# Kernel tuning notes

Hardware: AMD Instinct MI355X
Metric: run time of the kernel (lower is better)

Reference implementation:

```python
import jax, jax.numpy as jnp
import numpy as np

N, K, D_IN, D_H, D_A, N_CLS = 8192, 10, 1024, 512, 256, 4


def setup_inputs() -> dict:
    key = jax.random.key(0)
    ks = jax.random.split(key, 20)
    def lin(k, fan_in, shape):
        return jax.random.normal(k, shape, dtype=jnp.float32) / np.sqrt(fan_in)
    return {
        "x_path": jax.random.normal(ks[0], (N, D_IN), dtype=jnp.float32),
        "cluster_id": jax.random.randint(ks[1], (N,), 0, K),
        # per-cluster phi MLP (Linear 1024->512, ReLU, Linear 512->512, ReLU); dropout = eval identity
        "W1": lin(ks[2], D_IN, (K, D_IN, D_H)), "b1": jnp.zeros((K, D_H), jnp.float32),
        "W2": lin(ks[3], D_H, (K, D_H, D_H)), "b2": jnp.zeros((K, D_H), jnp.float32),
        # attention_net fc: Linear 512->512 + ReLU
        "fc_W": lin(ks[4], D_H, (D_H, D_H)), "fc_b": jnp.zeros((D_H,), jnp.float32),
        # Attn_Net_Gated: a=tanh(Va), b=sigmoid(Vb), A=(a*b)@Vc
        "Va": lin(ks[5], D_H, (D_H, D_A)), "ba": jnp.zeros((D_A,), jnp.float32),
        "Vb": lin(ks[6], D_H, (D_H, D_A)), "bb": jnp.zeros((D_A,), jnp.float32),
        "Vc": lin(ks[7], D_A, (D_A, 1)), "bc": jnp.zeros((1,), jnp.float32),
        # rho: Linear 512->256 + ReLU
        "rho_W": lin(ks[8], D_H, (D_H, D_A)), "rho_b": jnp.zeros((D_A,), jnp.float32),
        # classifier: Linear 256->4
        "cls_W": lin(ks[9], D_A, (D_A, N_CLS)), "cls_b": jnp.zeros((N_CLS,), jnp.float32),
    }


def reference(x_path, cluster_id, W1, b1, W2, b2, fc_W, fc_b,
              Va, ba, Vb, bb, Vc, bc, rho_W, rho_b, cls_W, cls_b):
    # mask[k, n] = 1 if patch n belongs to cluster k
    mask = (cluster_id[None, :] == jnp.arange(K)[:, None]).astype(x_path.dtype)  # [K, N]

    # per-cluster 2-layer MLP applied to all patches, masked mean-pool (= AdaptiveAvgPool1d(1))
    def phi(W1i, b1i, W2i, b2i):
        h = jax.nn.relu(x_path @ W1i + b1i)          # [N, 512]
        return jax.nn.relu(h @ W2i + b2i)            # [N, 512]
    y = jax.vmap(phi)(W1, b1, W2, b2)                # [K, N, 512]
    cnt = mask.sum(axis=1)                           # [K]
    pooled = jnp.einsum('kn,knd->kd', mask, y) / jnp.maximum(cnt, 1.0)[:, None]  # [K, 512]
    # empty cluster -> zeros (matches torch.zeros((1,512)) branch since b terms are zero via where)
    pooled = jnp.where(cnt[:, None] > 0, pooled, 0.0)

    # attention_net: fc + gated attention
    h = jax.nn.relu(pooled @ fc_W + fc_b)            # [K, 512]
    a = jnp.tanh(h @ Va + ba)                        # [K, 256]
    b = jax.nn.sigmoid(h @ Vb + bb)                  # [K, 256]
    A = (a * b) @ Vc + bc                            # [K, 1]
    A = jax.nn.softmax(A.T, axis=1)                  # [1, K]
    h_path = A @ h                                   # [1, 512]
    h_path = jax.nn.relu(h_path @ rho_W + rho_b)[0]  # [256]
    logits = (h_path @ cls_W + cls_b)[None, :]       # [1, 4]
    Y_hat = jnp.argmax(logits, axis=1, keepdims=True)
    hazards = jax.nn.sigmoid(logits)
    S = jnp.cumprod(1.0 - hazards, axis=1)
    return hazards, S, Y_hat
```

## Files before the change

kernel.cpp:

```cpp
#include <hip/hip_runtime.h>
#include <math.h>

#define NPATCH 8192
#define KC     10
#define DIN    1024
#define DH     512
#define DA     256
#define NCLS   4

#define TM  32
#define LDA 520

typedef unsigned short u16;
typedef short bf16x8 __attribute__((ext_vector_type(8)));
typedef float f32x4  __attribute__((ext_vector_type(4)));

#define OFF_CNT   0
#define OFF_IDX   64
#define OFF_PSUM  327744
#define OFF_H     348224
#define OFF_S     368704
#define OFF_H2    368768
#define OFF_W1P   369792
#define OFF_W2P   10855552
#define OFF_XB    16098432
#define OFF_H1    32875648

__device__ __forceinline__ u16 f2bf(float f) {
  union { float f; unsigned u; } v; v.f = f;
  unsigned r = (v.u + 0x7fffu + ((v.u >> 16) & 1u)) >> 16;
  return (u16)r;
}

struct __align__(8) U16x4 { u16 x, y, z, w; };

__device__ __forceinline__ void async16(const void* gp, void* lp) {
  __builtin_amdgcn_global_load_lds(
      (const __attribute__((address_space(1))) void*)gp,
      (__attribute__((address_space(3))) void*)lp, 16, 0, 0);
}

#define W1_TILES (KC * (DIN / 32) * (DH / 32))
#define W2_TILES (KC * (DH / 32) * (DH / 32))
#define NB_BUCKET 32
#define NB_XB     2048
#define NB_PREP   (NB_BUCKET + W1_TILES + W2_TILES + NB_XB)

__global__ __launch_bounds__(256) void prep_kernel(
    const int* __restrict__ cid, int* __restrict__ cnt,
    int* __restrict__ idxlist, const float* __restrict__ W1,
    const float* __restrict__ W2, u16* __restrict__ W1p,
    u16* __restrict__ W2p, const float* __restrict__ x,
    u16* __restrict__ xb, float* __restrict__ psum,
    float* __restrict__ sstore) {
  int b = blockIdx.x, t = threadIdx.x;
  if (b < NB_BUCKET) {
    int g = b * 256 + t;
    if (g < KC * DH) psum[g] = 0.f;
    if (g < KC) sstore[g] = 0.f;
    __shared__ int lcnt[KC], lbase[KC];
    if (t < KC) lcnt[t] = 0;
    __syncthreads();
    int n = b * 256 + t;
    int k = cid[n];
    int myoff = atomicAdd(&lcnt[k], 1);
    __syncthreads();
    if (t < KC) lbase[t] = atomicAdd(&cnt[t], lcnt[t]);
    __syncthreads();
    idxlist[k * NPATCH + lbase[k] + myoff] = n;
  } else if (b < NB_BUCKET + W1_TILES + W2_TILES) {
    __shared__ u16 tile[32][33];
    int bb = b - NB_BUCKET;
    const float* src;
    u16* dst;
    if (bb < W1_TILES) {
      int k = bb / 512, rem = bb % 512;
      int kb = rem / 16, n0 = (rem % 16) * 32;
      src = W1 + (size_t)k * DIN * DH + (size_t)kb * 32 * DH + n0;
      dst = W1p + (((size_t)(k * 32 + kb) * 512 + n0) * 32);
    } else {
      int b2 = bb - W1_TILES;
      int k = b2 / 256, rem = b2 % 256;
      int kb = rem / 16, n0 = (rem % 16) * 32;
      src = W2 + (size_t)k * DH * DH + (size_t)kb * 32 * DH + n0;
      dst = W2p + (((size_t)(k * 16 + kb) * 512 + n0) * 32);
    }
    {
      int ki = t >> 3, n4 = (t & 7) * 4;
      float4 v = *(const float4*)&src[(size_t)ki * DH + n4];
      tile[ki][n4 + 0] = f2bf(v.x);
      tile[ki][n4 + 1] = f2bf(v.y);
      tile[ki][n4 + 2] = f2bf(v.z);
      tile[ki][n4 + 3] = f2bf(v.w);
    }
    __syncthreads();
    {
      int n = t >> 3, ki = (t & 7) * 4;
      U16x4 o = {tile[ki + 0][n], tile[ki + 1][n], tile[ki + 2][n],
                 tile[ki + 3][n]};
      *(U16x4*)&dst[(size_t)n * 32 + ki] = o;
    }
  } else {
    int cb = b - (NB_BUCKET + W1_TILES + W2_TILES);
    size_t basei = (size_t)cb * 4096;
#pragma unroll
    for (int i = 0; i < 4; ++i) {
      size_t off = basei + (size_t)i * 1024 + (size_t)t * 4;
      float4 v = *(const float4*)(x + off);
      U16x4 o = {f2bf(v.x), f2bf(v.y), f2bf(v.z), f2bf(v.w)};
      *(U16x4*)(xb + off) = o;
    }
  }
}

__global__ __launch_bounds__(256) void phi1_kernel(
    const u16* __restrict__ xb, const u16* __restrict__ W1p,
    const float* __restrict__ b1, const int* __restrict__ cnt,
    const int* __restrict__ idxlist, u16* __restrict__ h1) {
  const int k = blockIdx.y;
  const int base = blockIdx.x * TM;
  const int nq = blockIdx.z;
  const int cntk = cnt[k];
  if (base >= cntk) return;

  const int tid = threadIdx.x;
  const int w = tid >> 6, lane = tid & 63;
  const int quad = lane >> 4, l16 = lane & 15;

  __shared__ __align__(16) u16 A_sh[TM * LDA];
  __shared__ int ridx[TM];
  if (tid < TM) {
    int r = base + tid;
    ridx[tid] = (r < cntk) ? idxlist[k * NPATCH + r] : -1;
  }
  __syncthreads();

  const f32x4 zero4 = {0.f, 0.f, 0.f, 0.f};
  f32x4 acc[2][2];
#pragma unroll
  for (int m = 0; m < 2; ++m)
#pragma unroll
    for (int nt = 0; nt < 2; ++nt) acc[m][nt] = zero4;

  for (int kh = 0; kh < 2; ++kh) {
    if (kh) __syncthreads();
    for (int rr = 0; rr < 8; ++rr) {
      int r = w * 8 + rr;
      int src = ridx[r];
      if (src >= 0) {
        async16(xb + (size_t)src * DIN + kh * 512 + lane * 8, &A_sh[r * LDA]);
      } else {
        bf16x8 z = {0, 0, 0, 0, 0, 0, 0, 0};
        *(bf16x8*)&A_sh[r * LDA + lane * 8] = z;
      }
    }
    __syncthreads();

    const u16* wb = W1p + ((size_t)(k * 32 + kh * 16) * 512 +
                           (nq * 128 + w * 32 + l16)) * 32 + quad * 8;
    bf16x8 B[2][8];
#pragma unroll
    for (int s = 0; s < 4; ++s)
#pragma unroll
      for (int nt = 0; nt < 2; ++nt)
        B[0][s * 2 + nt] = *(const bf16x8*)(wb + (size_t)s * 16384 + nt * 512);
#pragma unroll
    for (int g = 0; g < 4; ++g) {
      const int cur = g & 1, nxt = cur ^ 1;
      if (g < 3) {
#pragma unroll
        for (int s = 0; s < 4; ++s)
#pragma unroll
          for (int nt = 0; nt < 2; ++nt)
            B[nxt][s * 2 + nt] = *(const bf16x8*)(
                wb + (size_t)((g + 1) * 4 + s) * 16384 + nt * 512);
      }
#pragma unroll
      for (int s = 0; s < 4; ++s) {
        const int ks = g * 4 + s;
        bf16x8 af0 = *(const bf16x8*)&A_sh[l16 * LDA + ks * 32 + quad * 8];
        bf16x8 af1 =
            *(const bf16x8*)&A_sh[(16 + l16) * LDA + ks * 32 + quad * 8];
#pragma unroll
        for (int nt = 0; nt < 2; ++nt) {
          acc[0][nt] = __builtin_amdgcn_mfma_f32_16x16x32_bf16(
              af0, B[cur][s * 2 + nt], acc[0][nt], 0, 0, 0);
          acc[1][nt] = __builtin_amdgcn_mfma_f32_16x16x32_bf16(
              af1, B[cur][s * 2 + nt], acc[1][nt], 0, 0, 0);
        }
      }
    }
  }

  __syncthreads();
#pragma unroll
  for (int m = 0; m < 2; ++m)
#pragma unroll
    for (int nt = 0; nt < 2; ++nt) {
      int c = w * 32 + nt * 16 + l16;
      float bias = b1[k * DH + nq * 128 + c];
#pragma unroll
      for (int r = 0; r < 4; ++r) {
        int row = m * 16 + quad * 4 + r;
        A_sh[row * 136 + c] = f2bf(fmaxf(acc[m][nt][r] + bias, 0.f));
      }
    }
  __syncthreads();
  {
    int row = tid >> 3, seg = tid & 7;
    int n = ridx[row];
    if (n >= 0) {
      u16* dst = h1 + (size_t)n * DH + nq * 128 + seg * 16;
#pragma unroll
      for (int j = 0; j < 2; ++j)
        *(bf16x8*)(dst + j * 8) =
            *(const bf16x8*)&A_sh[row * 136 + seg * 16 + j * 8];
    }
  }
}

__global__ __launch_bounds__(256) void phi2_kernel(
    const u16* __restrict__ h1, const u16* __restrict__ W2p,
    const float* __restrict__ b2, const int* __restrict__ cnt,
    const int* __restrict__ idxlist, float* __restrict__ psum) {
  const int k = blockIdx.y;
  const int base = blockIdx.x * TM;
  const int nq = blockIdx.z;
  const int cntk = cnt[k];
  if (base >= cntk) return;

  const int tid = threadIdx.x;
  const int w = tid >> 6, lane = tid & 63;
  const int quad = lane >> 4, l16 = lane & 15;

  __shared__ __align__(16) u16 H_sh[TM * LDA];
  __shared__ int ridx[TM];
  if (tid < TM) {
    int r = base + tid;
    ridx[tid] = (r < cntk) ? idxlist[k * NPATCH + r] : -1;
  }
  __syncthreads();

  for (int rr = 0; rr < 8; ++rr) {
    int r = w * 8 + rr;
    int src = ridx[r];
    if (src >= 0) {
      async16(h1 + (size_t)src * DH + lane * 8, &H_sh[r * LDA]);
    } else {
      bf16x8 z = {0, 0, 0, 0, 0, 0, 0, 0};
      *(bf16x8*)&H_sh[r * LDA + lane * 8] = z;
    }
  }
  __syncthreads();

  const f32x4 zero4 = {0.f, 0.f, 0.f, 0.f};
  f32x4 acc[2][2];
#pragma unroll
  for (int m = 0; m < 2; ++m)
#pragma unroll
    for (int nt = 0; nt < 2; ++nt) acc[m][nt] = zero4;

  const u16* wb = W2p + ((size_t)(k * 16) * 512 +
                         (nq * 128 + w * 32 + l16)) * 32 + quad * 8;
  bf16x8 B[2][8];
#pragma unroll
  for (int s = 0; s < 4; ++s)
#pragma unroll
    for (int nt = 0; nt < 2; ++nt)
      B[0][s * 2 + nt] = *(const bf16x8*)(wb + (size_t)s * 16384 + nt * 512);
#pragma unroll
  for (int g = 0; g < 4; ++g) {
    const int cur = g & 1, nxt = cur ^ 1;
    if (g < 3) {
#pragma unroll
      for (int s = 0; s < 4; ++s)
#pragma unroll
        for (int nt = 0; nt < 2; ++nt)
          B[nxt][s * 2 + nt] = *(const bf16x8*)(
              wb + (size_t)((g + 1) * 4 + s) * 16384 + nt * 512);
    }
#pragma unroll
    for (int s = 0; s < 4; ++s) {
      const int ks = g * 4 + s;
      bf16x8 af0 = *(const bf16x8*)&H_sh[l16 * LDA + ks * 32 + quad * 8];
      bf16x8 af1 =
          *(const bf16x8*)&H_sh[(16 + l16) * LDA + ks * 32 + quad * 8];
#pragma unroll
      for (int nt = 0; nt < 2; ++nt) {
        acc[0][nt] = __builtin_amdgcn_mfma_f32_16x16x32_bf16(
            af0, B[cur][s * 2 + nt], acc[0][nt], 0, 0, 0);
        acc[1][nt] = __builtin_amdgcn_mfma_f32_16x16x32_bf16(
            af1, B[cur][s * 2 + nt], acc[1][nt], 0, 0, 0);
      }
    }
  }

  float vmask[2][4];
#pragma unroll
  for (int m = 0; m < 2; ++m)
#pragma unroll
    for (int r = 0; r < 4; ++r)
      vmask[m][r] = (ridx[m * 16 + quad * 4 + r] >= 0) ? 1.f : 0.f;

#pragma unroll
  for (int nt = 0; nt < 2; ++nt) {
    int col = nq * 128 + w * 32 + nt * 16 + l16;
    float bias = b2[k * DH + col];
    float s = 0.f;
#pragma unroll
    for (int m = 0; m < 2; ++m)
#pragma unroll
      for (int r = 0; r < 4; ++r)
        s += vmask[m][r] * fmaxf(acc[m][nt][r] + bias, 0.f);
    s += __shfl_xor(s, 16, 64);
    s += __shfl_xor(s, 32, 64);
    if (quad == 0) atomicAdd(&psum[k * DH + col], s);
  }
}

__global__ __launch_bounds__(256) void fc_kernel(
    const float* __restrict__ psum, const int* __restrict__ cnt,
    const float* __restrict__ fcW, const float* __restrict__ fcb,
    float* __restrict__ hstore) {
  __shared__ float p_sh[KC * DH];
  __shared__ float invs[16];
  __shared__ float red[16 * 16 * KC];
  const int tid = threadIdx.x;
  const int j0 = blockIdx.x * 16;
  const int j = tid & 15, dq = tid >> 4;

  if (tid < KC) {
    int c = cnt[tid];
    invs[tid] = (c > 0) ? 1.f / (float)c : 0.f;
  }
  __syncthreads();
#pragma unroll
  for (int it = 0; it < KC * DH / 256; ++it) {
    int e = it * 256 + tid;
    p_sh[e] = psum[e] * invs[e >> 9];
  }
  __syncthreads();

  float acc[KC];
#pragma unroll
  for (int k = 0; k < KC; ++k) acc[k] = 0.f;
#pragma unroll 8
  for (int i = 0; i < 32; ++i) {
    int ii = (i + dq) & 31;
    int d = dq * 32 + ii;
    float wv = fcW[(size_t)d * DH + j0 + j];
#pragma unroll
    for (int k = 0; k < KC; ++k)
      acc[k] = fmaf(p_sh[k * DH + d], wv, acc[k]);
  }
#pragma unroll
  for (int k = 0; k < KC; ++k) red[(dq * 16 + j) * KC + k] = acc[k];
  __syncthreads();
  if (tid < 16 * KC) {
    int jj = tid / KC, k = tid % KC;
    float s = 0.f;
#pragma unroll
    for (int q = 0; q < 16; ++q) s += red[(q * 16 + jj) * KC + k];
    hstore[k * DH + j0 + jj] = fmaxf(s + fcb[j0 + jj], 0.f);
  }
}

__global__ __launch_bounds__(256) void attn_kernel(
    const float* __restrict__ hstore, const float* __restrict__ Va,
    const float* __restrict__ ba, const float* __restrict__ Vb,
    const float* __restrict__ bb_, const float* __restrict__ Vc,
    float* __restrict__ sstore) {
  __shared__ float h_sh[KC * DH];
  __shared__ float reda[16 * 16 * KC];
  __shared__ float redb[16 * 16 * KC];
  __shared__ float gred[16 * KC];
  const int tid = threadIdx.x;
  const int j0 = blockIdx.x * 16;
  const int j = tid & 15, dq = tid >> 4;

#pragma unroll
  for (int it = 0; it < KC * DH / 256; ++it) {
    int e = it * 256 + tid;
    h_sh[e] = hstore[e];
  }
  __syncthreads();

  float sa[KC], sb[KC];
#pragma unroll
  for (int k = 0; k < KC; ++k) { sa[k] = 0.f; sb[k] = 0.f; }
#pragma unroll 8
  for (int i = 0; i < 32; ++i) {
    int ii = (i + dq) & 31;
    int d = dq * 32 + ii;
    float va = Va[(size_t)d * DA + j0 + j];
    float vb = Vb[(size_t)d * DA + j0 + j];
#pragma unroll
    for (int k = 0; k < KC; ++k) {
      float h = h_sh[k * DH + d];
      sa[k] = fmaf(h, va, sa[k]);
      sb[k] = fmaf(h, vb, sb[k]);
    }
  }
#pragma unroll
  for (int k = 0; k < KC; ++k) {
    reda[(dq * 16 + j) * KC + k] = sa[k];
    redb[(dq * 16 + j) * KC + k] = sb[k];
  }
  __syncthreads();
  if (tid < 16 * KC) {
    int jj = tid / KC, k = tid % KC;
    float ta = 0.f, tb = 0.f;
#pragma unroll
    for (int q = 0; q < 16; ++q) {
      ta += reda[(q * 16 + jj) * KC + k];
      tb += redb[(q * 16 + jj) * KC + k];
    }
    float a = tanhf(ta + ba[j0 + jj]);
    float b = 1.f / (1.f + expf(-(tb + bb_[j0 + jj])));
    gred[jj * KC + k] = a * b * Vc[j0 + jj];
  }
  __syncthreads();
  if (tid < KC) {
    float s = 0.f;
#pragma unroll
    for (int jj = 0; jj < 16; ++jj) s += gred[jj * KC + tid];
    atomicAdd(&sstore[tid], s);
  }
}

__global__ __launch_bounds__(256) void rho_kernel(
    const float* __restrict__ hstore, const float* __restrict__ sstore,
    const float* __restrict__ rhoW, const float* __restrict__ rhob,
    float* __restrict__ h2g) {
  __shared__ float ws_sh[KC];
  __shared__ float hp_sh[DH];
  __shared__ float red[8 * 32];
  const int tid = threadIdx.x;
  const int j0 = blockIdx.x * 32;
  const int j = tid & 31, dq = tid >> 5;

  if (tid == 0) {
    float sv[KC], m = -1e30f;
#pragma unroll
    for (int k = 0; k < KC; ++k) { sv[k] = sstore[k]; m = fmaxf(m, sv[k]); }
    float Z = 0.f;
#pragma unroll
    for (int k = 0; k < KC; ++k) { sv[k] = expf(sv[k] - m); Z += sv[k]; }
    float invZ = 1.f / Z;
#pragma unroll
    for (int k = 0; k < KC; ++k) ws_sh[k] = sv[k] * invZ;
  }
  __syncthreads();
#pragma unroll
  for (int it = 0; it < 2; ++it) {
    int d = it * 256 + tid;
    float s = 0.f;
#pragma unroll
    for (int k = 0; k < KC; ++k) s = fmaf(ws_sh[k], hstore[k * DH + d], s);
    hp_sh[d] = s;
  }
  __syncthreads();

  float acc = 0.f;
#pragma unroll 8
  for (int i = 0; i < 64; ++i) {
    int d = dq * 64 + i;
    acc = fmaf(hp_sh[d], rhoW[(size_t)d * DA + j0 + j], acc);
  }
  red[dq * 32 + j] = acc;
  __syncthreads();
  if (tid < 32) {
    float s = 0.f;
#pragma unroll
    for (int q = 0; q < 8; ++q) s += red[q * 32 + tid];
    h2g[j0 + tid] = fmaxf(s + rhob[j0 + tid], 0.f);
  }
}

__global__ __launch_bounds__(256) void cls_kernel(
    const float* __restrict__ h2g, const float* __restrict__ clsW,
    const float* __restrict__ clsb, float* __restrict__ out) {
  __shared__ float rd[NCLS][256];
  const int tid = threadIdx.x;
  float h = h2g[tid];
#pragma unroll
  for (int c = 0; c < NCLS; ++c) rd[c][tid] = h * clsW[tid * NCLS + c];
  __syncthreads();
  for (int s = 128; s > 0; s >>= 1) {
    if (tid < s) {
#pragma unroll
      for (int c = 0; c < NCLS; ++c) rd[c][tid] += rd[c][tid + s];
    }
    __syncthreads();
  }
  if (tid == 0) {
    float lg[NCLS], hz[NCLS];
    int best = 0;
#pragma unroll
    for (int c = 0; c < NCLS; ++c) {
      lg[c] = rd[c][0] + clsb[c];
      hz[c] = 1.f / (1.f + expf(-lg[c]));
      if (lg[c] > lg[best]) best = c;
    }
    float S = 1.f;
#pragma unroll
    for (int c = 0; c < NCLS; ++c) out[c] = hz[c];
#pragma unroll
    for (int c = 0; c < NCLS; ++c) {
      S *= (1.f - hz[c]);
      out[NCLS + c] = S;
    }
    out[2 * NCLS] = (float)best;
  }
}

extern "C" void kernel_launch(void* const* d_in, const int* in_sizes, int n_in,
                              void* d_out, int out_size, void* d_ws,
                              size_t ws_size, hipStream_t stream) {
  const float* x    = (const float*)d_in[0];
  const int*   cid  = (const int*)d_in[1];
  const float* W1   = (const float*)d_in[2];
  const float* b1   = (const float*)d_in[3];
  const float* W2   = (const float*)d_in[4];
  const float* b2   = (const float*)d_in[5];
  const float* fcW  = (const float*)d_in[6];
  const float* fcb  = (const float*)d_in[7];
  const float* Va   = (const float*)d_in[8];
  const float* ba   = (const float*)d_in[9];
  const float* Vb   = (const float*)d_in[10];
  const float* bb_  = (const float*)d_in[11];
  const float* Vc   = (const float*)d_in[12];
  const float* rhoW = (const float*)d_in[14];
  const float* rhob = (const float*)d_in[15];
  const float* clsW = (const float*)d_in[16];
  const float* clsb = (const float*)d_in[17];
  float* out = (float*)d_out;

  char* ws = (char*)d_ws;
  int*   cnt     = (int*)(ws + OFF_CNT);
  int*   idxlist = (int*)(ws + OFF_IDX);
  float* psum    = (float*)(ws + OFF_PSUM);
  float* hstore  = (float*)(ws + OFF_H);
  float* sstore  = (float*)(ws + OFF_S);
  float* h2g     = (float*)(ws + OFF_H2);
  u16*   W1p     = (u16*)(ws + OFF_W1P);
  u16*   W2p     = (u16*)(ws + OFF_W2P);
  u16*   xb      = (u16*)(ws + OFF_XB);
  u16*   h1      = (u16*)(ws + OFF_H1);

  (void)hipMemsetAsync(cnt, 0, 64, stream);
  prep_kernel<<<NB_PREP, 256, 0, stream>>>(cid, cnt, idxlist, W1, W2, W1p, W2p,
                                           x, xb, psum, sstore);
  phi1_kernel<<<dim3(NPATCH / TM, KC, 4), 256, 0, stream>>>(xb, W1p, b1, cnt,
                                                            idxlist, h1);
  phi2_kernel<<<dim3(NPATCH / TM, KC, 4), 256, 0, stream>>>(h1, W2p, b2, cnt,
                                                            idxlist, psum);
  fc_kernel<<<32, 256, 0, stream>>>(psum, cnt, fcW, fcb, hstore);
  attn_kernel<<<16, 256, 0, stream>>>(hstore, Va, ba, Vb, bb_, Vc, sstore);
  rho_kernel<<<8, 256, 0, stream>>>(hstore, sstore, rhoW, rhob, h2g);
  cls_kernel<<<1, 256, 0, stream>>>(h2g, clsW, clsb, out);
}
```

Baseline: 208.7 us.

## Fuse x conversion into phi1, widen GEMM N-tile, merge tail kernels with grid barrier

The separate fp32-to-bf16 pass over x is removed. phi1 now loads fp32 rows synchronously and converts them while staging into shared memory, which saves a full write and reread of x. The phi1 and phi2 GEMM tiles are widened from 128 to 256 output columns, halving the z grid and reusing each staged A tile across more MFMAs. The four small tail kernels (fc, attn, rho, cls) are merged into one 64-block kernel that uses atomic spin barriers in global memory, removing launch gaps. This relies on all 64 blocks being co-resident, and the barrier counters sit inside the 64-byte region cleared by the memset. The synchronous x loads also give up the earlier async-to-LDS path.

```diff
diff --git a/kernel.cpp b/kernel.cpp
--- a/kernel.cpp
+++ b/kernel.cpp
@@ -16,15 +16,15 @@
 typedef float f32x4  __attribute__((ext_vector_type(4)));
 
 #define OFF_CNT   0
+#define OFF_BAR   48
 #define OFF_IDX   64
 #define OFF_PSUM  327744
 #define OFF_H     348224
-#define OFF_S     368704
 #define OFF_H2    368768
-#define OFF_W1P   369792
-#define OFF_W2P   10855552
-#define OFF_XB    16098432
-#define OFF_H1    32875648
+#define OFF_SRED  369792
+#define OFF_W1P   373888
+#define OFF_W2P   10859648
+#define OFF_H1    16102528
 
 __device__ __forceinline__ u16 f2bf(float f) {
   union { float f; unsigned u; } v; v.f = f;
@@ -43,21 +43,17 @@
 #define W1_TILES (KC * (DIN / 32) * (DH / 32))
 #define W2_TILES (KC * (DH / 32) * (DH / 32))
 #define NB_BUCKET 32
-#define NB_XB     2048
-#define NB_PREP   (NB_BUCKET + W1_TILES + W2_TILES + NB_XB)
+#define NB_PREP (NB_BUCKET + W1_TILES + W2_TILES)
 
 __global__ __launch_bounds__(256) void prep_kernel(
     const int* __restrict__ cid, int* __restrict__ cnt,
     int* __restrict__ idxlist, const float* __restrict__ W1,
     const float* __restrict__ W2, u16* __restrict__ W1p,
-    u16* __restrict__ W2p, const float* __restrict__ x,
-    u16* __restrict__ xb, float* __restrict__ psum,
-    float* __restrict__ sstore) {
+    u16* __restrict__ W2p, float* __restrict__ psum) {
   int b = blockIdx.x, t = threadIdx.x;
   if (b < NB_BUCKET) {
     int g = b * 256 + t;
     if (g < KC * DH) psum[g] = 0.f;
-    if (g < KC) sstore[g] = 0.f;
     __shared__ int lcnt[KC], lbase[KC];
     if (t < KC) lcnt[t] = 0;
     __syncthreads();
@@ -68,7 +64,7 @@
     if (t < KC) lbase[t] = atomicAdd(&cnt[t], lcnt[t]);
     __syncthreads();
     idxlist[k * NPATCH + lbase[k] + myoff] = n;
-  } else if (b < NB_BUCKET + W1_TILES + W2_TILES) {
+  } else {
     __shared__ u16 tile[32][33];
     int bb = b - NB_BUCKET;
     const float* src;
@@ -100,21 +96,11 @@
                  tile[ki + 3][n]};
       *(U16x4*)&dst[(size_t)n * 32 + ki] = o;
     }
-  } else {
-    int cb = b - (NB_BUCKET + W1_TILES + W2_TILES);
-    size_t basei = (size_t)cb * 4096;
-#pragma unroll
-    for (int i = 0; i < 4; ++i) {
-      size_t off = basei + (size_t)i * 1024 + (size_t)t * 4;
-      float4 v = *(const float4*)(x + off);
-      U16x4 o = {f2bf(v.x), f2bf(v.y), f2bf(v.z), f2bf(v.w)};
-      *(U16x4*)(xb + off) = o;
-    }
   }
 }
 
 __global__ __launch_bounds__(256) void phi1_kernel(
-    const u16* __restrict__ xb, const u16* __restrict__ W1p,
+    const float* __restrict__ x, const u16* __restrict__ W1p,
     const float* __restrict__ b1, const int* __restrict__ cnt,
     const int* __restrict__ idxlist, u16* __restrict__ h1) {
   const int k = blockIdx.y;
@@ -136,57 +122,63 @@
   __syncthreads();
 
   const f32x4 zero4 = {0.f, 0.f, 0.f, 0.f};
-  f32x4 acc[2][2];
+  f32x4 acc[2][4];
 #pragma unroll
   for (int m = 0; m < 2; ++m)
 #pragma unroll
-    for (int nt = 0; nt < 2; ++nt) acc[m][nt] = zero4;
+    for (int nt = 0; nt < 4; ++nt) acc[m][nt] = zero4;
 
   for (int kh = 0; kh < 2; ++kh) {
     if (kh) __syncthreads();
+#pragma unroll
     for (int rr = 0; rr < 8; ++rr) {
       int r = w * 8 + rr;
       int src = ridx[r];
+      bf16x8 o = {0, 0, 0, 0, 0, 0, 0, 0};
       if (src >= 0) {
-        async16(xb + (size_t)src * DIN + kh * 512 + lane * 8, &A_sh[r * LDA]);
-      } else {
-        bf16x8 z = {0, 0, 0, 0, 0, 0, 0, 0};
-        *(bf16x8*)&A_sh[r * LDA + lane * 8] = z;
-      }
+        const float4* xp =
+            (const float4*)(x + (size_t)src * DIN + kh * 512 + lane * 8);
+        float4 v0 = xp[0], v1 = xp[1];
+        o[0] = (short)f2bf(v0.x); o[1] = (short)f2bf(v0.y);
+        o[2] = (short)f2bf(v0.z); o[3] = (short)f2bf(v0.w);
+        o[4] = (short)f2bf(v1.x); o[5] = (short)f2bf(v1.y);
+        o[6] = (short)f2bf(v1.z); o[7] = (short)f2bf(v1.w);
+      }
+      *(bf16x8*)&A_sh[r * LDA + lane * 8] = o;
     }
     __syncthreads();
 
     const u16* wb = W1p + ((size_t)(k * 32 + kh * 16) * 512 +
-                           (nq * 128 + w * 32 + l16)) * 32 + quad * 8;
+                           (nq * 256 + w * 64 + l16)) * 32 + quad * 8;
     bf16x8 B[2][8];
 #pragma unroll
-    for (int s = 0; s < 4; ++s)
-#pragma unroll
-      for (int nt = 0; nt < 2; ++nt)
-        B[0][s * 2 + nt] = *(const bf16x8*)(wb + (size_t)s * 16384 + nt * 512);
-#pragma unroll
-    for (int g = 0; g < 4; ++g) {
+    for (int s = 0; s < 2; ++s)
+#pragma unroll
+      for (int nt = 0; nt < 4; ++nt)
+        B[0][s * 4 + nt] = *(const bf16x8*)(wb + (size_t)s * 16384 + nt * 512);
+#pragma unroll
+    for (int g = 0; g < 8; ++g) {
       const int cur = g & 1, nxt = cur ^ 1;
-      if (g < 3) {
-#pragma unroll
-        for (int s = 0; s < 4; ++s)
-#pragma unroll
-          for (int nt = 0; nt < 2; ++nt)
-            B[nxt][s * 2 + nt] = *(const bf16x8*)(
-                wb + (size_t)((g + 1) * 4 + s) * 16384 + nt * 512);
-      }
-#pragma unroll
-      for (int s = 0; s < 4; ++s) {
-        const int ks = g * 4 + s;
+      if (g < 7) {
+#pragma unroll
+        for (int s = 0; s < 2; ++s)
+#pragma unroll
+          for (int nt = 0; nt < 4; ++nt)
+            B[nxt][s * 4 + nt] = *(const bf16x8*)(
+                wb + (size_t)((g + 1) * 2 + s) * 16384 + nt * 512);
+      }
+#pragma unroll
+      for (int s = 0; s < 2; ++s) {
+        const int ks = g * 2 + s;
         bf16x8 af0 = *(const bf16x8*)&A_sh[l16 * LDA + ks * 32 + quad * 8];
         bf16x8 af1 =
             *(const bf16x8*)&A_sh[(16 + l16) * LDA + ks * 32 + quad * 8];
 #pragma unroll
-        for (int nt = 0; nt < 2; ++nt) {
+        for (int nt = 0; nt < 4; ++nt) {
           acc[0][nt] = __builtin_amdgcn_mfma_f32_16x16x32_bf16(
-              af0, B[cur][s * 2 + nt], acc[0][nt], 0, 0, 0);
+              af0, B[cur][s * 4 + nt], acc[0][nt], 0, 0, 0);
           acc[1][nt] = __builtin_amdgcn_mfma_f32_16x16x32_bf16(
-              af1, B[cur][s * 2 + nt], acc[1][nt], 0, 0, 0);
+              af1, B[cur][s * 4 + nt], acc[1][nt], 0, 0, 0);
         }
       }
     }
@@ -196,13 +188,13 @@
 #pragma unroll
   for (int m = 0; m < 2; ++m)
 #pragma unroll
-    for (int nt = 0; nt < 2; ++nt) {
-      int c = w * 32 + nt * 16 + l16;
-      float bias = b1[k * DH + nq * 128 + c];
+    for (int nt = 0; nt < 4; ++nt) {
+      int c = w * 64 + nt * 16 + l16;
+      float bias = b1[k * DH + nq * 256 + c];
 #pragma unroll
       for (int r = 0; r < 4; ++r) {
         int row = m * 16 + quad * 4 + r;
-        A_sh[row * 136 + c] = f2bf(fmaxf(acc[m][nt][r] + bias, 0.f));
+        A_sh[row * 264 + c] = f2bf(fmaxf(acc[m][nt][r] + bias, 0.f));
       }
     }
   __syncthreads();
@@ -210,11 +202,11 @@
     int row = tid >> 3, seg = tid & 7;
     int n = ridx[row];
     if (n >= 0) {
-      u16* dst = h1 + (size_t)n * DH + nq * 128 + seg * 16;
-#pragma unroll
-      for (int j = 0; j < 2; ++j)
+      u16* dst = h1 + (size_t)n * DH + nq * 256 + seg * 32;
+#pragma unroll
+      for (int j = 0; j < 4; ++j)
         *(bf16x8*)(dst + j * 8) =
-            *(const bf16x8*)&A_sh[row * 136 + seg * 16 + j * 8];
+            *(const bf16x8*)&A_sh[row * 264 + seg * 32 + j * 8];
     }
   }
 }
@@ -254,43 +246,43 @@
   __syncthreads();
 
   const f32x4 zero4 = {0.f, 0.f, 0.f, 0.f};
-  f32x4 acc[2][2];
+  f32x4 acc[2][4];
 #pragma unroll
   for (int m = 0; m < 2; ++m)
 #pragma unroll
-    for (int nt = 0; nt < 2; ++nt) acc[m][nt] = zero4;
+    for (int nt = 0; nt < 4; ++nt) acc[m][nt] = zero4;
 
   const u16* wb = W2p + ((size_t)(k * 16) * 512 +
-                         (nq * 128 + w * 32 + l16)) * 32 + quad * 8;
+                         (nq * 256 + w * 64 + l16)) * 32 + quad * 8;
   bf16x8 B[2][8];
 #pragma unroll
-  for (int s = 0; s < 4; ++s)
-#pragma unroll
-    for (int nt = 0; nt < 2; ++nt)
-      B[0][s * 2 + nt] = *(const bf16x8*)(wb + (size_t)s * 16384 + nt * 512);
-#pragma unroll
-  for (int g = 0; g < 4; ++g) {
+  for (int s = 0; s < 2; ++s)
+#pragma unroll
+    for (int nt = 0; nt < 4; ++nt)
+      B[0][s * 4 + nt] = *(const bf16x8*)(wb + (size_t)s * 16384 + nt * 512);
+#pragma unroll
+  for (int g = 0; g < 8; ++g) {
     const int cur = g & 1, nxt = cur ^ 1;
-    if (g < 3) {
-#pragma unroll
-      for (int s = 0; s < 4; ++s)
-#pragma unroll
-        for (int nt = 0; nt < 2; ++nt)
-          B[nxt][s * 2 + nt] = *(const bf16x8*)(
-              wb + (size_t)((g + 1) * 4 + s) * 16384 + nt * 512);
-    }
-#pragma unroll
-    for (int s = 0; s < 4; ++s) {
-      const int ks = g * 4 + s;
+    if (g < 7) {
+#pragma unroll
+      for (int s = 0; s < 2; ++s)
+#pragma unroll
+        for (int nt = 0; nt < 4; ++nt)
+          B[nxt][s * 4 + nt] = *(const bf16x8*)(
+              wb + (size_t)((g + 1) * 2 + s) * 16384 + nt * 512);
+    }
+#pragma unroll
+    for (int s = 0; s < 2; ++s) {
+      const int ks = g * 2 + s;
       bf16x8 af0 = *(const bf16x8*)&H_sh[l16 * LDA + ks * 32 + quad * 8];
       bf16x8 af1 =
           *(const bf16x8*)&H_sh[(16 + l16) * LDA + ks * 32 + quad * 8];
 #pragma unroll
-      for (int nt = 0; nt < 2; ++nt) {
+      for (int nt = 0; nt < 4; ++nt) {
         acc[0][nt] = __builtin_amdgcn_mfma_f32_16x16x32_bf16(
-            af0, B[cur][s * 2 + nt], acc[0][nt], 0, 0, 0);
+            af0, B[cur][s * 4 + nt], acc[0][nt], 0, 0, 0);
         acc[1][nt] = __builtin_amdgcn_mfma_f32_16x16x32_bf16(
-            af1, B[cur][s * 2 + nt], acc[1][nt], 0, 0, 0);
+            af1, B[cur][s * 4 + nt], acc[1][nt], 0, 0, 0);
       }
     }
   }
@@ -303,8 +295,8 @@
       vmask[m][r] = (ridx[m * 16 + quad * 4 + r] >= 0) ? 1.f : 0.f;
 
 #pragma unroll
-  for (int nt = 0; nt < 2; ++nt) {
-    int col = nq * 128 + w * 32 + nt * 16 + l16;
+  for (int nt = 0; nt < 4; ++nt) {
+    int col = nq * 256 + w * 64 + nt * 16 + l16;
     float bias = b2[k * DH + col];
     float s = 0.f;
 #pragma unroll
@@ -318,16 +310,40 @@
   }
 }
 
-__global__ __launch_bounds__(256) void fc_kernel(
+#define NTB 64
+
+__device__ __forceinline__ void bar_arrive_wait(int* bar) {
+  __syncthreads();
+  if (threadIdx.x == 0) {
+    __threadfence();
+    __hip_atomic_fetch_add(bar, 1, __ATOMIC_RELEASE, __HIP_MEMORY_SCOPE_AGENT);
+    while (__hip_atomic_load(bar, __ATOMIC_ACQUIRE,
+                             __HIP_MEMORY_SCOPE_AGENT) < NTB) {
+      __builtin_amdgcn_s_sleep(1);
+    }
+  }
+  __syncthreads();
+}
+
+__global__ __launch_bounds__(256) void tail_kernel(
     const float* __restrict__ psum, const int* __restrict__ cnt,
     const float* __restrict__ fcW, const float* __restrict__ fcb,
-    float* __restrict__ hstore) {
+    const float* __restrict__ Va, const float* __restrict__ ba,
+    const float* __restrict__ Vb, const float* __restrict__ bb_,
+    const float* __restrict__ Vc, const float* __restrict__ rhoW,
+    const float* __restrict__ rhob, const float* __restrict__ clsW,
+    const float* __restrict__ clsb, float* __restrict__ hstore,
+    float* __restrict__ sred, float* __restrict__ h2g,
+    int* __restrict__ bar, float* __restrict__ out) {
   __shared__ float p_sh[KC * DH];
-  __shared__ float invs[16];
-  __shared__ float red[16 * 16 * KC];
+  __shared__ float r1[2560];
+  __shared__ float r2[2560];
+  __shared__ float invs[KC];
+  __shared__ float gate_sh[4 * KC];
+  __shared__ float ws_sh[KC];
+  __shared__ float hp_sh[DH];
   const int tid = threadIdx.x;
-  const int j0 = blockIdx.x * 16;
-  const int j = tid & 15, dq = tid >> 4;
+  const int b = blockIdx.x;
 
   if (tid < KC) {
     int c = cnt[tid];
@@ -340,115 +356,104 @@
     p_sh[e] = psum[e] * invs[e >> 9];
   }
   __syncthreads();
-
-  float acc[KC];
-#pragma unroll
-  for (int k = 0; k < KC; ++k) acc[k] = 0.f;
-#pragma unroll 8
-  for (int i = 0; i < 32; ++i) {
-    int ii = (i + dq) & 31;
-    int d = dq * 32 + ii;
-    float wv = fcW[(size_t)d * DH + j0 + j];
-#pragma unroll
-    for (int k = 0; k < KC; ++k)
-      acc[k] = fmaf(p_sh[k * DH + d], wv, acc[k]);
-  }
-#pragma unroll
-  for (int k = 0; k < KC; ++k) red[(dq * 16 + j) * KC + k] = acc[k];
-  __syncthreads();
-  if (tid < 16 * KC) {
-    int jj = tid / KC, k = tid % KC;
-    float s = 0.f;
-#pragma unroll
-    for (int q = 0; q < 16; ++q) s += red[(q * 16 + jj) * KC + k];
-    hstore[k * DH + j0 + jj] = fmaxf(s + fcb[j0 + jj], 0.f);
-  }
-}
-
-__global__ __launch_bounds__(256) void attn_kernel(
-    const float* __restrict__ hstore, const float* __restrict__ Va,
-    const float* __restrict__ ba, const float* __restrict__ Vb,
-    const float* __restrict__ bb_, const float* __restrict__ Vc,
-    float* __restrict__ sstore) {
-  __shared__ float h_sh[KC * DH];
-  __shared__ float reda[16 * 16 * KC];
-  __shared__ float redb[16 * 16 * KC];
-  __shared__ float gred[16 * KC];
-  const int tid = threadIdx.x;
-  const int j0 = blockIdx.x * 16;
-  const int j = tid & 15, dq = tid >> 4;
+  {
+    const int jj = tid & 7, dq = tid >> 3;
+    const int j0 = b * 8;
+    float acc[KC];
+#pragma unroll
+    for (int k = 0; k < KC; ++k) acc[k] = 0.f;
+#pragma unroll 4
+    for (int i = 0; i < 16; ++i) {
+      int d = dq * 16 + i;
+      float wv = fcW[(size_t)d * DH + j0 + jj];
+#pragma unroll
+      for (int k = 0; k < KC; ++k) acc[k] = fmaf(p_sh[k * DH + d], wv, acc[k]);
+    }
+#pragma unroll
+    for (int k = 0; k < KC; ++k) r1[(dq * 8 + jj) * KC + k] = acc[k];
+    __syncthreads();
+    if (tid < 8 * KC) {
+      int jj2 = tid / KC, k = tid % KC;
+      float s = 0.f;
+#pragma unroll
+      for (int q = 0; q < 32; ++q) s += r1[(q * 8 + jj2) * KC + k];
+      hstore[k * DH + j0 + jj2] = fmaxf(s + fcb[j0 + jj2], 0.f);
+    }
+  }
+  bar_arrive_wait(&bar[0]);
 
 #pragma unroll
   for (int it = 0; it < KC * DH / 256; ++it) {
     int e = it * 256 + tid;
-    h_sh[e] = hstore[e];
-  }
-  __syncthreads();
-
-  float sa[KC], sb[KC];
-#pragma unroll
-  for (int k = 0; k < KC; ++k) { sa[k] = 0.f; sb[k] = 0.f; }
-#pragma unroll 8
-  for (int i = 0; i < 32; ++i) {
-    int ii = (i + dq) & 31;
-    int d = dq * 32 + ii;
-    float va = Va[(size_t)d * DA + j0 + j];
-    float vb = Vb[(size_t)d * DA + j0 + j];
+    p_sh[e] = hstore[e];
+  }
+  __syncthreads();
+  {
+    const int jj = tid & 3, dq = tid >> 2;
+    const int j0 = b * 4;
+    float sa[KC], sb[KC];
+#pragma unroll
+    for (int k = 0; k < KC; ++k) { sa[k] = 0.f; sb[k] = 0.f; }
+#pragma unroll 4
+    for (int i = 0; i < 8; ++i) {
+      int d = dq * 8 + i;
+      float va = Va[(size_t)d * DA + j0 + jj];
+      float vb = Vb[(size_t)d * DA + j0 + jj];
+#pragma unroll
+      for (int k = 0; k < KC; ++k) {
+        float h = p_sh[k * DH + d];
+        sa[k] = fmaf(h, va, sa[k]);
+        sb[k] = fmaf(h, vb, sb[k]);
+      }
+    }
 #pragma unroll
     for (int k = 0; k < KC; ++k) {
-      float h = h_sh[k * DH + d];
-      sa[k] = fmaf(h, va, sa[k]);
-      sb[k] = fmaf(h, vb, sb[k]);
-    }
-  }
-#pragma unroll
-  for (int k = 0; k < KC; ++k) {
-    reda[(dq * 16 + j) * KC + k] = sa[k];
-    redb[(dq * 16 + j) * KC + k] = sb[k];
-  }
-  __syncthreads();
-  if (tid < 16 * KC) {
-    int jj = tid / KC, k = tid % KC;
-    float ta = 0.f, tb = 0.f;
-#pragma unroll
-    for (int q = 0; q < 16; ++q) {
-      ta += reda[(q * 16 + jj) * KC + k];
-      tb += redb[(q * 16 + jj) * KC + k];
-    }
-    float a = tanhf(ta + ba[j0 + jj]);
-    float b = 1.f / (1.f + expf(-(tb + bb_[j0 + jj])));
-    gred[jj * KC + k] = a * b * Vc[j0 + jj];
-  }
-  __syncthreads();
+      r1[(dq * 4 + jj) * KC + k] = sa[k];
+      r2[(dq * 4 + jj) * KC + k] = sb[k];
+    }
+    __syncthreads();
+    if (tid < 4 * KC) {
+      int jj2 = tid / KC, k = tid % KC;
+      float ta = 0.f, tb = 0.f;
+#pragma unroll
+      for (int q = 0; q < 64; ++q) {
+        ta += r1[(q * 4 + jj2) * KC + k];
+        tb += r2[(q * 4 + jj2) * KC + k];
+      }
+      float a = tanhf(ta + ba[j0 + jj2]);
+      float g = 1.f / (1.f + expf(-(tb + bb_[j0 + jj2])));
+      gate_sh[jj2 * KC + k] = a * g * Vc[j0 + jj2];
+    }
+    __syncthreads();
+    if (tid < KC) {
+      float s = 0.f;
+#pragma unroll
+      for (int jj2 = 0; jj2 < 4; ++jj2) s += gate_sh[jj2 * KC + tid];
+      sred[b * 16 + tid] = s;
+    }
+  }
+  bar_arrive_wait(&bar[1]);
+
   if (tid < KC) {
     float s = 0.f;
-#pragma unroll
-    for (int jj = 0; jj < 16; ++jj) s += gred[jj * KC + tid];
-    atomicAdd(&sstore[tid], s);
-  }
-}
-
-__global__ __launch_bounds__(256) void rho_kernel(
-    const float* __restrict__ hstore, const float* __restrict__ sstore,
-    const float* __restrict__ rhoW, const float* __restrict__ rhob,
-    float* __restrict__ h2g) {
-  __shared__ float ws_sh[KC];
-  __shared__ float hp_sh[DH];
-  __shared__ float red[8 * 32];
-  const int tid = threadIdx.x;
-  const int j0 = blockIdx.x * 32;
-  const int j = tid & 31, dq = tid >> 5;
-
+    for (int q = 0; q < NTB; ++q) s += sred[q * 16 + tid];
+    ws_sh[tid] = s;
+  }
+  __syncthreads();
   if (tid == 0) {
-    float sv[KC], m = -1e30f;
-#pragma unroll
-    for (int k = 0; k < KC; ++k) { sv[k] = sstore[k]; m = fmaxf(m, sv[k]); }
+    float m = -1e30f;
+#pragma unroll
+    for (int k2 = 0; k2 < KC; ++k2) m = fmaxf(m, ws_sh[k2]);
     float Z = 0.f;
 #pragma unroll
-    for (int k = 0; k < KC; ++k) { sv[k] = expf(sv[k] - m); Z += sv[k]; }
-    float invZ = 1.f / Z;
-#pragma unroll
-    for (int k = 0; k < KC; ++k) ws_sh[k] = sv[k] * invZ;
+    for (int k2 = 0; k2 < KC; ++k2) {
+      float e = expf(ws_sh[k2] - m);
+      ws_sh[k2] = e;
+      Z += e;
+    }
+    float iZ = 1.f / Z;
+#pragma unroll
+    for (int k2 = 0; k2 < KC; ++k2) ws_sh[k2] *= iZ;
   }
   __syncthreads();
 #pragma unroll
@@ -456,61 +461,72 @@
     int d = it * 256 + tid;
     float s = 0.f;
 #pragma unroll
-    for (int k = 0; k < KC; ++k) s = fmaf(ws_sh[k], hstore[k * DH + d], s);
+    for (int k2 = 0; k2 < KC; ++k2) s = fmaf(ws_sh[k2], p_sh[k2 * DH + d], s);
     hp_sh[d] = s;
   }
   __syncthreads();
-
-  float acc = 0.f;
-#pragma unroll 8
-  for (int i = 0; i < 64; ++i) {
-    int d = dq * 64 + i;
-    acc = fmaf(hp_sh[d], rhoW[(size_t)d * DA + j0 + j], acc);
-  }
-  red[dq * 32 + j] = acc;
-  __syncthreads();
-  if (tid < 32) {
-    float s = 0.f;
-#pragma unroll
-    for (int q = 0; q < 8; ++q) s += red[q * 32 + tid];
-    h2g[j0 + tid] = fmaxf(s + rhob[j0 + tid], 0.f);
-  }
-}
-
-__global__ __launch_bounds__(256) void cls_kernel(
-    const float* __restrict__ h2g, const float* __restrict__ clsW,
-    const float* __restrict__ clsb, float* __restrict__ out) {
-  __shared__ float rd[NCLS][256];
-  const int tid = threadIdx.x;
-  float h = h2g[tid];
-#pragma unroll
-  for (int c = 0; c < NCLS; ++c) rd[c][tid] = h * clsW[tid * NCLS + c];
-  __syncthreads();
-  for (int s = 128; s > 0; s >>= 1) {
-    if (tid < s) {
-#pragma unroll
-      for (int c = 0; c < NCLS; ++c) rd[c][tid] += rd[c][tid + s];
-    }
-    __syncthreads();
-  }
-  if (tid == 0) {
-    float lg[NCLS], hz[NCLS];
-    int best = 0;
-#pragma unroll
-    for (int c = 0; c < NCLS; ++c) {
-      lg[c] = rd[c][0] + clsb[c];
-      hz[c] = 1.f / (1.f + expf(-lg[c]));
-      if (lg[c] > lg[best]) best = c;
-    }
-    float S = 1.f;
-#pragma unroll
-    for (int c = 0; c < NCLS; ++c) out[c] = hz[c];
-#pragma unroll
-    for (int c = 0; c < NCLS; ++c) {
-      S *= (1.f - hz[c]);
-      out[NCLS + c] = S;
-    }
-    out[2 * NCLS] = (float)best;
+  {
+    const int jj = tid & 3, dq = tid >> 2;
+    const int j0 = b * 4;
+    float acc = 0.f;
+#pragma unroll 4
+    for (int i = 0; i < 8; ++i) {
+      int d = dq * 8 + i;
+      acc = fmaf(hp_sh[d], rhoW[(size_t)d * DA + j0 + jj], acc);
+    }
+    r1[dq * 4 + jj] = acc;
+    __syncthreads();
+    if (tid < 4) {
+      float s = 0.f;
+#pragma unroll
+      for (int q = 0; q < 64; ++q) s += r1[q * 4 + tid];
+      h2g[j0 + tid] = fmaxf(s + rhob[j0 + tid], 0.f);
+    }
+  }
+
+  if (b != 0) {
+    __syncthreads();
+    if (tid == 0) {
+      __threadfence();
+      __hip_atomic_fetch_add(&bar[2], 1, __ATOMIC_RELEASE,
+                             __HIP_MEMORY_SCOPE_AGENT);
+    }
+    return;
+  }
+  bar_arrive_wait(&bar[2]);
+  {
+    float h = h2g[tid];
+#pragma unroll
+    for (int c = 0; c < NCLS; ++c)
+      r1[c * 256 + tid] = h * clsW[(size_t)tid * NCLS + c];
+    __syncthreads();
+    for (int s = 128; s > 0; s >>= 1) {
+      if (tid < s) {
+#pragma unroll
+        for (int c = 0; c < NCLS; ++c)
+          r1[c * 256 + tid] += r1[c * 256 + tid + s];
+      }
+      __syncthreads();
+    }
+    if (tid == 0) {
+      float lg[NCLS], hz[NCLS];
+      int best = 0;
+#pragma unroll
+      for (int c = 0; c < NCLS; ++c) {
+        lg[c] = r1[c * 256] + clsb[c];
+        hz[c] = 1.f / (1.f + expf(-lg[c]));
+        if (lg[c] > lg[best]) best = c;
+      }
+      float S = 1.f;
+#pragma unroll
+      for (int c = 0; c < NCLS; ++c) out[c] = hz[c];
+#pragma unroll
+      for (int c = 0; c < NCLS; ++c) {
+        S *= (1.f - hz[c]);
+        out[NCLS + c] = S;
+      }
+      out[2 * NCLS] = (float)best;
+    }
   }
 }
 
@@ -538,25 +554,24 @@
 
   char* ws = (char*)d_ws;
   int*   cnt     = (int*)(ws + OFF_CNT);
+  int*   bar     = (int*)(ws + OFF_BAR);
   int*   idxlist = (int*)(ws + OFF_IDX);
   float* psum    = (float*)(ws + OFF_PSUM);
   float* hstore  = (float*)(ws + OFF_H);
-  float* sstore  = (float*)(ws + OFF_S);
   float* h2g     = (float*)(ws + OFF_H2);
+  float* sred    = (float*)(ws + OFF_SRED);
   u16*   W1p     = (u16*)(ws + OFF_W1P);
   u16*   W2p     = (u16*)(ws + OFF_W2P);
-  u16*   xb      = (u16*)(ws + OFF_XB);
   u16*   h1      = (u16*)(ws + OFF_H1);
 
   (void)hipMemsetAsync(cnt, 0, 64, stream);
   prep_kernel<<<NB_PREP, 256, 0, stream>>>(cid, cnt, idxlist, W1, W2, W1p, W2p,
-                                           x, xb, psum, sstore);
-  phi1_kernel<<<dim3(NPATCH / TM, KC, 4), 256, 0, stream>>>(xb, W1p, b1, cnt,
+                                           psum);
+  phi1_kernel<<<dim3(NPATCH / TM, KC, 2), 256, 0, stream>>>(x, W1p, b1, cnt,
                                                             idxlist, h1);
-  phi2_kernel<<<dim3(NPATCH / TM, KC, 4), 256, 0, stream>>>(h1, W2p, b2, cnt,
+  phi2_kernel<<<dim3(NPATCH / TM, KC, 2), 256, 0, stream>>>(h1, W2p, b2, cnt,
                                                             idxlist, psum);
-  fc_kernel<<<32, 256, 0, stream>>>(psum, cnt, fcW, fcb, hstore);
-  attn_kernel<<<16, 256, 0, stream>>>(hstore, Va, ba, Vb, bb_, Vc, sstore);
-  rho_kernel<<<8, 256, 0, stream>>>(hstore, sstore, rhoW, rhob, h2g);
-  cls_kernel<<<1, 256, 0, stream>>>(h2g, clsW, clsb, out);
-}
+  tail_kernel<<<NTB, 256, 0, stream>>>(psum, cnt, fcW, fcb, Va, ba, Vb, bb_,
+                                       Vc, rhoW, rhob, clsW, clsb, hstore,
+                                       sred, h2g, bar, out);
+}
```

Measured after the change: 215.2 us. +3.1%, slower.
